# Performance work log

Hardware: AMD Instinct MI355X
Metric: run time of the kernel (lower is better)

## Reference

```python
import jax, jax.numpy as jnp
import numpy as np

N_HEAD = 16


def setup_inputs() -> dict:
    key = jax.random.key(0)
    ks = jax.random.split(key, 9)
    b, s, d = 4, 2048, 1024
    scale = 1.0 / np.sqrt(d)
    return {
        "x": jax.random.normal(ks[0], (b, s, d), dtype=jnp.float32),
        "Wq": jax.random.normal(ks[1], (d, d), dtype=jnp.float32) * scale,
        "bq": jax.random.normal(ks[2], (d,), dtype=jnp.float32) * 0.01,
        "Wk": jax.random.normal(ks[3], (d, d), dtype=jnp.float32) * scale,
        "bk": jax.random.normal(ks[4], (d,), dtype=jnp.float32) * 0.01,
        "Wv": jax.random.normal(ks[5], (d, d), dtype=jnp.float32) * scale,
        "bv": jax.random.normal(ks[6], (d,), dtype=jnp.float32) * 0.01,
        "Wo": jax.random.normal(ks[7], (d, d), dtype=jnp.float32) * scale,
        "bo": jax.random.normal(ks[8], (d,), dtype=jnp.float32) * 0.01,
        "mask": 1,
    }


def reference(x, Wq, bq, Wk, bk, Wv, bv, Wo, bo, mask):
    b, s, d = x.shape
    h = N_HEAD
    dh = d // h
    # projections -> [b, h, s, dh]
    def proj(W, bias):
        return (x @ W + bias).reshape(b, s, h, dh).transpose(0, 2, 1, 3)

    Q = proj(Wq, bq)
    K = proj(Wk, bk)
    V = proj(Wv, bv)

    # full S x S scores (module materializes them explicitly)
    scores = jnp.einsum('bhqd,bhkd->bhqk', Q, K)
    if mask:
        causal = jnp.triu(jnp.ones((s, s), dtype=bool), k=1)
        scores = jnp.where(causal, -jnp.inf, scores)
    scores = scores / jnp.sqrt(jnp.asarray(dh, dtype=scores.dtype))
    attn = jax.nn.softmax(scores, axis=-1)
    out = jnp.einsum('bhqk,bhkd->bhqd', attn, V)  # [b, h, s, dh]
    out = out.transpose(0, 2, 1, 3).reshape(b, s, d)
    return out @ Wo + bo
```

## Files before the change

### kernel.cpp

```cpp
#include <hip/hip_runtime.h>

typedef unsigned short u16;
typedef unsigned int u32;
typedef __bf16 bf16x8 __attribute__((ext_vector_type(8)));
typedef float f32x4 __attribute__((ext_vector_type(4)));

#define BATCH 4
#define SLEN 2048
#define DMODEL 1024
#define NHEAD 16
#define DHEAD 64
#define MROWS (BATCH * SLEN)

__device__ __forceinline__ u16 f32_to_bf16(float f) {
  u32 u = __float_as_uint(f);
  u32 r = (u + 0x7FFFu + ((u >> 16) & 1u)) >> 16;
  return (u16)r;
}
__device__ __forceinline__ u32 pack_bf16x2(float a, float b) {
  return (u32)f32_to_bf16(a) | ((u32)f32_to_bf16(b) << 16);
}

__device__ __forceinline__ u32 pack_trunc(float lo, float hi) {
#if __has_builtin(__builtin_amdgcn_perm)
  return __builtin_amdgcn_perm(__float_as_uint(hi), __float_as_uint(lo), 0x07060302u);
#else
  return (__float_as_uint(hi) & 0xFFFF0000u) | (__float_as_uint(lo) >> 16);
#endif
}
__device__ __forceinline__ u32 pack_round(float lo, float hi) {
  u32 ul = __float_as_uint(lo) + 0x8000u;
  u32 uh = __float_as_uint(hi) + 0x8000u;
#if __has_builtin(__builtin_amdgcn_perm)
  return __builtin_amdgcn_perm(uh, ul, 0x07060302u);
#else
  return (uh & 0xFFFF0000u) | (ul >> 16);
#endif
}

#if __has_builtin(__builtin_amdgcn_exp2f)
#define EXP2(x) __builtin_amdgcn_exp2f(x)
#else
#define EXP2(x) exp2f(x)
#endif

typedef const __attribute__((address_space(1))) void* gas_cv;
typedef __attribute__((address_space(3))) void* las_v;
__device__ __forceinline__ void async16(const u16* g, u16* l) {
  __builtin_amdgcn_global_load_lds((gas_cv)g, (las_v)l, 16, 0, 0);
}


__global__ void convert_x_kernel(const float* __restrict__ x, u16* __restrict__ xb) {
  size_t i = ((size_t)blockIdx.x * 256 + threadIdx.x) * 8;
  float4 v0 = *(const float4*)(x + i);
  float4 v1 = *(const float4*)(x + i + 4);
  uint4 o;
  o.x = pack_bf16x2(v0.x, v0.y);
  o.y = pack_bf16x2(v0.z, v0.w);
  o.z = pack_bf16x2(v1.x, v1.y);
  o.w = pack_bf16x2(v1.z, v1.w);
  *(uint4*)(xb + i) = o;
}

__global__ void transpose_w_kernel(const float* __restrict__ Wq, const float* __restrict__ Wk,
                                   const float* __restrict__ Wv, const float* __restrict__ Wo,
                                   u16* __restrict__ wqkvt, u16* __restrict__ wot) {
  __shared__ float tile[32][33];
  int z = blockIdx.z;
  const float* src = (z == 0) ? Wq : (z == 1) ? Wk : (z == 2) ? Wv : Wo;
  u16* dst = (z < 3) ? (wqkvt + (size_t)z * DMODEL * DMODEL) : wot;
  int c0 = blockIdx.x * 32, r0 = blockIdx.y * 32;
  int tx = threadIdx.x & 31, ty = threadIdx.x >> 5;
#pragma unroll
  for (int i = 0; i < 4; ++i)
    tile[ty + 8 * i][tx] = src[(size_t)(r0 + ty + 8 * i) * DMODEL + c0 + tx];
  __syncthreads();
#pragma unroll
  for (int i = 0; i < 4; ++i)
    dst[(size_t)(c0 + ty + 8 * i) * DMODEL + r0 + tx] = f32_to_bf16(tile[tx][ty + 8 * i]);
}

__global__ void concat_bias_kernel(const float* __restrict__ bq, const float* __restrict__ bk,
                                   const float* __restrict__ bv, float* __restrict__ bqkv) {
  int i = blockIdx.x * 256 + threadIdx.x;
  float v = (i < 1024) ? bq[i] : (i < 2048) ? bk[i - 1024] : bv[i - 2048];
  bqkv[i] = v;
}

__global__ void transpose_v_kernel(const u16* __restrict__ qkv, u16* __restrict__ vt) {
  __shared__ u16 tile[32][33];
  const int bh = blockIdx.z;
  const int b = bh >> 4, h = bh & 15;
  const int s0 = blockIdx.x * 32, d0 = blockIdx.y * 32;
  const int tx = threadIdx.x & 31, ty = threadIdx.x >> 5;
#pragma unroll
  for (int i = 0; i < 4; ++i)
    tile[ty + 8 * i][tx] =
        qkv[(size_t)(b * SLEN + s0 + ty + 8 * i) * (3 * DMODEL) + 2 * DMODEL + h * DHEAD + d0 + tx];
  __syncthreads();
#pragma unroll
  for (int i = 0; i < 4; ++i)
    vt[(size_t)(bh * DHEAD + d0 + ty + 8 * i) * SLEN + s0 + tx] = tile[tx][ty + 8 * i];
}

template <int OUT_BF16>
__global__ __launch_bounds__(256) void gemm_bt_kernel(const u16* __restrict__ A,
                                                      const u16* __restrict__ Bt,
                                                      const float* __restrict__ bias,
                                                      void* __restrict__ Cout,
                                                      int M, int N, int K) {
  __shared__ u16 sA[128 * 32];
  __shared__ u16 sB[128 * 32];
  const int tid = threadIdx.x;
  const int wv = tid >> 6, lane = tid & 63;
  const int wr = wv >> 1, wc = wv & 1;
  const int col = lane & 15, quad = lane >> 4;
  const int m0 = blockIdx.x * 128;
  const int n0 = blockIdx.y * 128;

  f32x4 acc[4][4] = {};

  const int lr = tid >> 2;
  const int ls = tid & 3;
  const size_t a_base = (size_t)(m0 + lr) * K + ls * 8;
  const size_t b_base = (size_t)(n0 + lr) * K + ls * 8;
  u16* ldsA0 = sA + ((tid >> 6) << 9);
  u16* ldsA1 = ldsA0 + 2048;
  u16* ldsB0 = sB + ((tid >> 6) << 9);
  u16* ldsB1 = ldsB0 + 2048;

  for (int k0 = 0; k0 < K; k0 += 32) {
    async16(A + a_base + k0, ldsA0);
    async16(A + a_base + (size_t)64 * K + k0, ldsA1);
    async16(Bt + b_base + k0, ldsB0);
    async16(Bt + b_base + (size_t)64 * K + k0, ldsB1);
    __syncthreads();
    bf16x8 af[4], bfr[4];
#pragma unroll
    for (int i = 0; i < 4; ++i)
      af[i] = *(const bf16x8*)(sA + (wr * 64 + i * 16 + col) * 32 + quad * 8);
#pragma unroll
    for (int j = 0; j < 4; ++j)
      bfr[j] = *(const bf16x8*)(sB + (wc * 64 + j * 16 + col) * 32 + quad * 8);
#pragma unroll
    for (int i = 0; i < 4; ++i)
#pragma unroll
      for (int j = 0; j < 4; ++j)
        acc[i][j] = __builtin_amdgcn_mfma_f32_16x16x32_bf16(af[i], bfr[j], acc[i][j], 0, 0, 0);
    __syncthreads();
  }

#pragma unroll
  for (int i = 0; i < 4; ++i) {
#pragma unroll
    for (int j = 0; j < 4; ++j) {
      int n = n0 + wc * 64 + j * 16 + col;
      float bia = bias[n];
#pragma unroll
      for (int r = 0; r < 4; ++r) {
        int m = m0 + wr * 64 + i * 16 + quad * 4 + r;
        float v = acc[i][j][r] + bia;
        if (OUT_BF16)
          ((u16*)Cout)[(size_t)m * N + n] = f32_to_bf16(v);
        else
          ((float*)Cout)[(size_t)m * N + n] = v;
      }
    }
  }
}

__global__ __launch_bounds__(256, 2) void attn_kernel(const u16* __restrict__ qkv,
                                                      const u16* __restrict__ vt,
                                                      u16* __restrict__ out) {
  const int bh = blockIdx.y;
  const int b = bh >> 4, h = bh & 15;
  const int tid = threadIdx.x;
  const int wv = tid >> 6, lane = tid & 63;
  const int col = lane & 15, quad = lane >> 4;
  const int bx = blockIdx.x;
  const int sfirst = bx * 4 + wv;

  __shared__ u16 sK[2][64 * 64];
  __shared__ u16 sV[2][64 * 64];
  __shared__ u16 sP[4][32 * 72];
  u16* mysP = sP[wv];

  const u16* kbase = qkv + ((size_t)(b * SLEN)) * (3 * DMODEL) + DMODEL + h * DHEAD;
  const u16* vbase = vt + ((size_t)bh * DHEAD) * SLEN;
  const float scl2 = 0.125f * 1.44269504088896f;

  const int lrow = lane >> 3;
  const int sga = (lane & 7) ^ lrow;
  const int r0a = wv * 16, r0b = wv * 16 + 8;
  const int swz = ((quad ) ^ (col & 7)) * 8;

  for (int half = 0; half < 2; ++half) {
    const int s2 = half ? (63 - sfirst) : sfirst;
    const int qbase = s2 * 32;
    const int nt_own = s2 / 2 + 1;
    const int nt_max = half ? (32 - 2 * bx) : (2 * bx + 2);

    const u16* qrow = qkv + ((size_t)(b * SLEN + qbase + col)) * (3 * DMODEL) + h * DHEAD;
    bf16x8 aQ[2][2];
#pragma unroll
    for (int i = 0; i < 2; ++i)
#pragma unroll
      for (int ks = 0; ks < 2; ++ks)
        aQ[i][ks] = *(const bf16x8*)(qrow + (size_t)i * 16 * (3 * DMODEL) + ks * 32 + quad * 8);

    f32x4 accO[2][4] = {};
    float m2[2] = {-1e30f, -1e30f}, l_i[2] = {0.0f, 0.0f};

    async16(kbase + (size_t)(r0a + lrow) * (3 * DMODEL) + sga * 8, sK[0] + r0a * 64);
    async16(kbase + (size_t)(r0b + lrow) * (3 * DMODEL) + sga * 8, sK[0] + r0b * 64);
    async16(vbase + (size_t)(r0a + lrow) * SLEN + sga * 8, sV[0] + r0a * 64);
    async16(vbase + (size_t)(r0b + lrow) * SLEN + sga * 8, sV[0] + r0b * 64);
    __syncthreads();

    for (int t = 0; t < nt_max; ++t) {
      const int kv0 = t * 64;
      const int cur = t & 1, nxt = cur ^ 1;

      if (t + 1 < nt_max) {
        const int kvn = kv0 + 64;
        async16(kbase + (size_t)(kvn + r0a + lrow) * (3 * DMODEL) + sga * 8, sK[nxt] + r0a * 64);
        async16(kbase + (size_t)(kvn + r0b + lrow) * (3 * DMODEL) + sga * 8, sK[nxt] + r0b * 64);
        async16(vbase + (size_t)(r0a + lrow) * SLEN + kvn + sga * 8, sV[nxt] + r0a * 64);
        async16(vbase + (size_t)(r0b + lrow) * SLEN + kvn + sga * 8, sV[nxt] + r0b * 64);
      }

      if (t < nt_own) {
        const u16* sKc = sK[cur];
        const u16* sVc = sV[cur];
        bf16x8 bK[2][4], bV[2][4];
#pragma unroll
        for (int ks = 0; ks < 2; ++ks) {
          const int sl = (((ks * 4 + quad) ^ (col & 7)) * 8);
#pragma unroll
          for (int cb = 0; cb < 4; ++cb)
            bK[ks][cb] = *(const bf16x8*)(sKc + (cb * 16 + col) * 64 + sl);
#pragma unroll
          for (int j = 0; j < 4; ++j)
            bV[ks][j] = *(const bf16x8*)(sVc + (j * 16 + col) * 64 + sl);
        }

        f32x4 accST[2][4] = {};
#pragma unroll
        for (int ks = 0; ks < 2; ++ks)
#pragma unroll
          for (int cb = 0; cb < 4; ++cb)
#pragma unroll
            for (int i = 0; i < 2; ++i)
              accST[i][cb] = __builtin_amdgcn_mfma_f32_16x16x32_bf16(bK[ks][cb], aQ[i][ks],
                                                                    accST[i][cb], 0, 0, 0);

        if (t == nt_own - 1) {
#pragma unroll
          for (int i = 0; i < 2; ++i) {
            int q = qbase + i * 16 + col;
#pragma unroll
            for (int cb = 0; cb < 4; ++cb) {
              int kvb = kv0 + cb * 16 + quad * 4;
#pragma unroll
              for (int r = 0; r < 4; ++r)
                if (kvb + r > q) accST[i][cb][r] = -1e30f;
            }
          }
        }

        float rmax[2], mnew[2], alpha[2], rsum[2];
#pragma unroll
        for (int i = 0; i < 2; ++i) {
          float m = accST[i][0][0];
#pragma unroll
          for (int cb = 0; cb < 4; ++cb)
#pragma unroll
            for (int r = 0; r < 4; ++r) m = fmaxf(m, accST[i][cb][r]);
          rmax[i] = m;
        }
#pragma unroll
        for (int i = 0; i < 2; ++i) {
          rmax[i] = fmaxf(rmax[i], __shfl_xor(rmax[i], 16));
          rmax[i] = fmaxf(rmax[i], __shfl_xor(rmax[i], 32));
          mnew[i] = fmaxf(m2[i], rmax[i] * scl2);
          alpha[i] = EXP2(m2[i] - mnew[i]);
          m2[i] = mnew[i];
        }
#pragma unroll
        for (int i = 0; i < 2; ++i) {
          float sacc = 0.0f;
#pragma unroll
          for (int cb = 0; cb < 4; ++cb)
#pragma unroll
            for (int r = 0; r < 4; ++r) {
              float p = EXP2(__builtin_fmaf(accST[i][cb][r], scl2, -mnew[i]));
              accST[i][cb][r] = p;
              sacc += p;
            }
          rsum[i] = sacc;
        }
#pragma unroll
        for (int i = 0; i < 2; ++i) {
          rsum[i] += __shfl_xor(rsum[i], 16);
          rsum[i] += __shfl_xor(rsum[i], 32);
          l_i[i] = l_i[i] * alpha[i] + rsum[i];
        }
#pragma unroll
        for (int i = 0; i < 2; ++i)
#pragma unroll
          for (int j = 0; j < 4; ++j)
#pragma unroll
            for (int r = 0; r < 4; ++r) accO[i][j][r] *= alpha[i];

#pragma unroll
        for (int i = 0; i < 2; ++i)
#pragma unroll
          for (int cb = 0; cb < 4; ++cb) {
            uint2 pk;
            pk.x = pack_trunc(accST[i][cb][0], accST[i][cb][1]);
            pk.y = pack_trunc(accST[i][cb][2], accST[i][cb][3]);
            *(uint2*)(mysP + (i * 16 + col) * 72 + cb * 16 + quad * 4) = pk;
          }
        bf16x8 aP[2][2];
#pragma unroll
        for (int i = 0; i < 2; ++i)
#pragma unroll
          for (int ks = 0; ks < 2; ++ks)
            aP[i][ks] = *(const bf16x8*)(mysP + (i * 16 + col) * 72 + ks * 32 + quad * 8);

#pragma unroll
        for (int ks = 0; ks < 2; ++ks)
#pragma unroll
          for (int j = 0; j < 4; ++j)
#pragma unroll
            for (int i = 0; i < 2; ++i)
              accO[i][j] = __builtin_amdgcn_mfma_f32_16x16x32_bf16(bV[ks][j], aP[i][ks],
                                                                  accO[i][j], 0, 0, 0);
      }

      __syncthreads();
    }

#pragma unroll
    for (int i = 0; i < 2; ++i) {
      float rl = 1.0f / l_i[i];
      size_t rowoff = ((size_t)(b * SLEN + qbase + i * 16 + col)) * DMODEL + h * DHEAD;
#pragma unroll
      for (int j = 0; j < 4; ++j) {
        uint2 pk;
        pk.x = pack_round(accO[i][j][0] * rl, accO[i][j][1] * rl);
        pk.y = pack_round(accO[i][j][2] * rl, accO[i][j][3] * rl);
        *(uint2*)(out + rowoff + j * 16 + quad * 4) = pk;
      }
    }
  }
}


extern "C" void kernel_launch(void* const* d_in, const int* in_sizes, int n_in,
                              void* d_out, int out_size, void* d_ws, size_t ws_size,
                              hipStream_t stream) {
  const float* x = (const float*)d_in[0];
  const float* Wq = (const float*)d_in[1];
  const float* bq = (const float*)d_in[2];
  const float* Wk = (const float*)d_in[3];
  const float* bk = (const float*)d_in[4];
  const float* Wv = (const float*)d_in[5];
  const float* bv = (const float*)d_in[6];
  const float* Wo = (const float*)d_in[7];
  const float* bo = (const float*)d_in[8];

  char* ws = (char*)d_ws;
  u16* xb = (u16*)ws;
  u16* wqkvt = (u16*)(ws + ((size_t)16 << 20));
  u16* wot = (u16*)(ws + ((size_t)22 << 20));
  u16* qkv = (u16*)(ws + ((size_t)24 << 20));
  u16* attnO = (u16*)(ws + ((size_t)72 << 20));
  float* bqkv = (float*)(ws + ((size_t)88 << 20));
  u16* vtp = xb;

  convert_x_kernel<<<4096, 256, 0, stream>>>(x, xb);
  transpose_w_kernel<<<dim3(32, 32, 4), 256, 0, stream>>>(Wq, Wk, Wv, Wo, wqkvt, wot);
  concat_bias_kernel<<<12, 256, 0, stream>>>(bq, bk, bv, bqkv);
  gemm_bt_kernel<1><<<dim3(64, 24), 256, 0, stream>>>(xb, wqkvt, bqkv, (void*)qkv,
                                                      MROWS, 3 * DMODEL, DMODEL);
  transpose_v_kernel<<<dim3(64, 2, 64), 256, 0, stream>>>(qkv, vtp);
  attn_kernel<<<dim3(8, BATCH * NHEAD), 256, 0, stream>>>(qkv, vtp, attnO);
  gemm_bt_kernel<0><<<dim3(64, 8), 256, 0, stream>>>(attnO, wot, bo, d_out,
                                                     MROWS, DMODEL, DMODEL);
}
```

Before: 286.3 us.

## Fuse V transpose into QKV GEMM epilogue, widen GEMM K-tile, re-split attention grid

The QKV projection GEMM now writes Q and K to a 2048-wide buffer and writes V directly in transposed per-head layout from its epilogue. This removes the separate transpose kernel and its extra read and write of V. The GEMM K-step grows from 32 to 64 and uses XOR-swizzled LDS to cut barriers and bank conflicts. Attention drops its two-half causal load balancing in favour of 16 blocks per head, launched heaviest-first with a launch-bounds hint of 3. This may lose load balance and adds register pressure.

```diff
diff --git a/kernel.cpp b/kernel.cpp
--- a/kernel.cpp
+++ b/kernel.cpp
@@ -11,6 +11,7 @@
 #define NHEAD 16
 #define DHEAD 64
 #define MROWS (BATCH * SLEN)
+#define QKS 2048
 
 __device__ __forceinline__ u16 f32_to_bf16(float f) {
   u32 u = __float_as_uint(f);
@@ -88,66 +89,49 @@
   bqkv[i] = v;
 }
 
-__global__ void transpose_v_kernel(const u16* __restrict__ qkv, u16* __restrict__ vt) {
-  __shared__ u16 tile[32][33];
-  const int bh = blockIdx.z;
-  const int b = bh >> 4, h = bh & 15;
-  const int s0 = blockIdx.x * 32, d0 = blockIdx.y * 32;
-  const int tx = threadIdx.x & 31, ty = threadIdx.x >> 5;
-#pragma unroll
-  for (int i = 0; i < 4; ++i)
-    tile[ty + 8 * i][tx] =
-        qkv[(size_t)(b * SLEN + s0 + ty + 8 * i) * (3 * DMODEL) + 2 * DMODEL + h * DHEAD + d0 + tx];
-  __syncthreads();
-#pragma unroll
-  for (int i = 0; i < 4; ++i)
-    vt[(size_t)(bh * DHEAD + d0 + ty + 8 * i) * SLEN + s0 + tx] = tile[tx][ty + 8 * i];
-}
-
-template <int OUT_BF16>
+
+#define GEMM_STAGE(Aptr, Bptr, k0)                                                     \
+  _Pragma("unroll") for (int c = 0; c < 4; ++c) {                                      \
+    const int rr = wv * 32 + c * 8;                                                    \
+    async16(Aptr + (size_t)(m0 + rr + lrow8) * K + (k0) + sga * 8, sA + rr * 64);      \
+    async16(Bptr + (size_t)(n0 + rr + lrow8) * K + (k0) + sga * 8, sB + rr * 64);      \
+  }
+
+#define GEMM_COMPUTE()                                                                 \
+  _Pragma("unroll") for (int ks = 0; ks < 2; ++ks) {                                   \
+    const int sl = ((ks * 4 + quad) ^ (col & 7)) * 8;                                  \
+    bf16x8 af[4], bfr[4];                                                              \
+    _Pragma("unroll") for (int i = 0; i < 4; ++i)                                      \
+        af[i] = *(const bf16x8*)(sA + (wr * 64 + i * 16 + col) * 64 + sl);             \
+    _Pragma("unroll") for (int j = 0; j < 4; ++j)                                      \
+        bfr[j] = *(const bf16x8*)(sB + (wc * 64 + j * 16 + col) * 64 + sl);            \
+    _Pragma("unroll") for (int i = 0; i < 4; ++i)                                      \
+        _Pragma("unroll") for (int j = 0; j < 4; ++j)                                  \
+            acc[i][j] = __builtin_amdgcn_mfma_f32_16x16x32_bf16(af[i], bfr[j],         \
+                                                                acc[i][j], 0, 0, 0);  \
+  }
+
 __global__ __launch_bounds__(256) void gemm_bt_kernel(const u16* __restrict__ A,
                                                       const u16* __restrict__ Bt,
                                                       const float* __restrict__ bias,
-                                                      void* __restrict__ Cout,
+                                                      float* __restrict__ Cout,
                                                       int M, int N, int K) {
-  __shared__ u16 sA[128 * 32];
-  __shared__ u16 sB[128 * 32];
+  __shared__ u16 sA[128 * 64];
+  __shared__ u16 sB[128 * 64];
   const int tid = threadIdx.x;
   const int wv = tid >> 6, lane = tid & 63;
   const int wr = wv >> 1, wc = wv & 1;
   const int col = lane & 15, quad = lane >> 4;
+  const int lrow8 = lane >> 3, sga = (lane & 7) ^ lrow8;
   const int m0 = blockIdx.x * 128;
   const int n0 = blockIdx.y * 128;
 
   f32x4 acc[4][4] = {};
 
-  const int lr = tid >> 2;
-  const int ls = tid & 3;
-  const size_t a_base = (size_t)(m0 + lr) * K + ls * 8;
-  const size_t b_base = (size_t)(n0 + lr) * K + ls * 8;
-  u16* ldsA0 = sA + ((tid >> 6) << 9);
-  u16* ldsA1 = ldsA0 + 2048;
-  u16* ldsB0 = sB + ((tid >> 6) << 9);
-  u16* ldsB1 = ldsB0 + 2048;
-
-  for (int k0 = 0; k0 < K; k0 += 32) {
-    async16(A + a_base + k0, ldsA0);
-    async16(A + a_base + (size_t)64 * K + k0, ldsA1);
-    async16(Bt + b_base + k0, ldsB0);
-    async16(Bt + b_base + (size_t)64 * K + k0, ldsB1);
+  for (int k0 = 0; k0 < K; k0 += 64) {
+    GEMM_STAGE(A, Bt, k0)
     __syncthreads();
-    bf16x8 af[4], bfr[4];
-#pragma unroll
-    for (int i = 0; i < 4; ++i)
-      af[i] = *(const bf16x8*)(sA + (wr * 64 + i * 16 + col) * 32 + quad * 8);
-#pragma unroll
-    for (int j = 0; j < 4; ++j)
-      bfr[j] = *(const bf16x8*)(sB + (wc * 64 + j * 16 + col) * 32 + quad * 8);
-#pragma unroll
-    for (int i = 0; i < 4; ++i)
-#pragma unroll
-      for (int j = 0; j < 4; ++j)
-        acc[i][j] = __builtin_amdgcn_mfma_f32_16x16x32_bf16(af[i], bfr[j], acc[i][j], 0, 0, 0);
+    GEMM_COMPUTE()
     __syncthreads();
   }
 
@@ -160,17 +144,72 @@
 #pragma unroll
       for (int r = 0; r < 4; ++r) {
         int m = m0 + wr * 64 + i * 16 + quad * 4 + r;
-        float v = acc[i][j][r] + bia;
-        if (OUT_BF16)
-          ((u16*)Cout)[(size_t)m * N + n] = f32_to_bf16(v);
-        else
-          ((float*)Cout)[(size_t)m * N + n] = v;
-      }
-    }
-  }
-}
-
-__global__ __launch_bounds__(256, 2) void attn_kernel(const u16* __restrict__ qkv,
+        Cout[(size_t)m * N + n] = acc[i][j][r] + bia;
+      }
+    }
+  }
+}
+
+__global__ __launch_bounds__(256) void gemm_qkv_kernel(const u16* __restrict__ A,
+                                                       const u16* __restrict__ Bt,
+                                                       const float* __restrict__ bias,
+                                                       u16* __restrict__ qk,
+                                                       u16* __restrict__ vt) {
+  const int K = DMODEL;
+  __shared__ u16 sA[128 * 64];
+  __shared__ u16 sB[128 * 64];
+  const int tid = threadIdx.x;
+  const int wv = tid >> 6, lane = tid & 63;
+  const int wr = wv >> 1, wc = wv & 1;
+  const int col = lane & 15, quad = lane >> 4;
+  const int lrow8 = lane >> 3, sga = (lane & 7) ^ lrow8;
+  const int m0 = blockIdx.x * 128;
+  const int n0 = blockIdx.y * 128;
+
+  f32x4 acc[4][4] = {};
+
+  for (int k0 = 0; k0 < K; k0 += 64) {
+    GEMM_STAGE(A, Bt, k0)
+    __syncthreads();
+    GEMM_COMPUTE()
+    __syncthreads();
+  }
+
+  if (n0 < 2048) {
+#pragma unroll
+    for (int i = 0; i < 4; ++i) {
+#pragma unroll
+      for (int j = 0; j < 4; ++j) {
+        int n = n0 + wc * 64 + j * 16 + col;
+        float bia = bias[n];
+#pragma unroll
+        for (int r = 0; r < 4; ++r) {
+          int m = m0 + wr * 64 + i * 16 + quad * 4 + r;
+          qk[(size_t)m * QKS + n] = f32_to_bf16(acc[i][j][r] + bia);
+        }
+      }
+    }
+  } else {
+#pragma unroll
+    for (int i = 0; i < 4; ++i) {
+      int m = m0 + wr * 64 + i * 16 + quad * 4;
+      int b = m >> 11, s = m & 2047;
+#pragma unroll
+      for (int j = 0; j < 4; ++j) {
+        int n = n0 + wc * 64 + j * 16 + col;
+        float bia = bias[n];
+        int hd = n - 2048;
+        size_t off = (size_t)((b << 10) | hd) * SLEN + s;
+        uint2 pk;
+        pk.x = pack_round(acc[i][j][0] + bia, acc[i][j][1] + bia);
+        pk.y = pack_round(acc[i][j][2] + bia, acc[i][j][3] + bia);
+        *(uint2*)(vt + off) = pk;
+      }
+    }
+  }
+}
+
+__global__ __launch_bounds__(256, 3) void attn_kernel(const u16* __restrict__ qk,
                                                       const u16* __restrict__ vt,
                                                       u16* __restrict__ out) {
   const int bh = blockIdx.y;
@@ -178,181 +217,176 @@
   const int tid = threadIdx.x;
   const int wv = tid >> 6, lane = tid & 63;
   const int col = lane & 15, quad = lane >> 4;
-  const int bx = blockIdx.x;
-  const int sfirst = bx * 4 + wv;
+  const int bxr = 15 - (int)blockIdx.x;
+  const int s2 = bxr * 4 + wv;
+  const int qbase = s2 * 32;
+  const int nt_own = s2 / 2 + 1;
+  const int nt_max = 2 * bxr + 2;
 
   __shared__ u16 sK[2][64 * 64];
   __shared__ u16 sV[2][64 * 64];
   __shared__ u16 sP[4][32 * 72];
   u16* mysP = sP[wv];
 
-  const u16* kbase = qkv + ((size_t)(b * SLEN)) * (3 * DMODEL) + DMODEL + h * DHEAD;
+  const u16* kbase = qk + ((size_t)(b * SLEN)) * QKS + 1024 + h * DHEAD;
   const u16* vbase = vt + ((size_t)bh * DHEAD) * SLEN;
   const float scl2 = 0.125f * 1.44269504088896f;
 
   const int lrow = lane >> 3;
   const int sga = (lane & 7) ^ lrow;
   const int r0a = wv * 16, r0b = wv * 16 + 8;
-  const int swz = ((quad ) ^ (col & 7)) * 8;
-
-  for (int half = 0; half < 2; ++half) {
-    const int s2 = half ? (63 - sfirst) : sfirst;
-    const int qbase = s2 * 32;
-    const int nt_own = s2 / 2 + 1;
-    const int nt_max = half ? (32 - 2 * bx) : (2 * bx + 2);
-
-    const u16* qrow = qkv + ((size_t)(b * SLEN + qbase + col)) * (3 * DMODEL) + h * DHEAD;
-    bf16x8 aQ[2][2];
-#pragma unroll
-    for (int i = 0; i < 2; ++i)
+
+  const u16* qrow = qk + ((size_t)(b * SLEN + qbase + col)) * QKS + h * DHEAD;
+  bf16x8 aQ[2][2];
+#pragma unroll
+  for (int i = 0; i < 2; ++i)
+#pragma unroll
+    for (int ks = 0; ks < 2; ++ks)
+      aQ[i][ks] = *(const bf16x8*)(qrow + (size_t)i * 16 * QKS + ks * 32 + quad * 8);
+
+  f32x4 accO[2][4] = {};
+  float m2[2] = {-1e30f, -1e30f}, l_i[2] = {0.0f, 0.0f};
+
+  async16(kbase + (size_t)(r0a + lrow) * QKS + sga * 8, sK[0] + r0a * 64);
+  async16(kbase + (size_t)(r0b + lrow) * QKS + sga * 8, sK[0] + r0b * 64);
+  async16(vbase + (size_t)(r0a + lrow) * SLEN + sga * 8, sV[0] + r0a * 64);
+  async16(vbase + (size_t)(r0b + lrow) * SLEN + sga * 8, sV[0] + r0b * 64);
+  __syncthreads();
+
+  for (int t = 0; t < nt_max; ++t) {
+    const int kv0 = t * 64;
+    const int cur = t & 1, nxt = cur ^ 1;
+
+    if (t + 1 < nt_max) {
+      const int kvn = kv0 + 64;
+      async16(kbase + (size_t)(kvn + r0a + lrow) * QKS + sga * 8, sK[nxt] + r0a * 64);
+      async16(kbase + (size_t)(kvn + r0b + lrow) * QKS + sga * 8, sK[nxt] + r0b * 64);
+      async16(vbase + (size_t)(r0a + lrow) * SLEN + kvn + sga * 8, sV[nxt] + r0a * 64);
+      async16(vbase + (size_t)(r0b + lrow) * SLEN + kvn + sga * 8, sV[nxt] + r0b * 64);
+    }
+
+    if (t < nt_own) {
+      const u16* sKc = sK[cur];
+      const u16* sVc = sV[cur];
+      bf16x8 bK[2][4], bV[2][4];
+#pragma unroll
+      for (int ks = 0; ks < 2; ++ks) {
+        const int sl = (((ks * 4 + quad) ^ (col & 7)) * 8);
+#pragma unroll
+        for (int cb = 0; cb < 4; ++cb)
+          bK[ks][cb] = *(const bf16x8*)(sKc + (cb * 16 + col) * 64 + sl);
+#pragma unroll
+        for (int j = 0; j < 4; ++j)
+          bV[ks][j] = *(const bf16x8*)(sVc + (j * 16 + col) * 64 + sl);
+      }
+
+      f32x4 accST[2][4] = {};
 #pragma unroll
       for (int ks = 0; ks < 2; ++ks)
-        aQ[i][ks] = *(const bf16x8*)(qrow + (size_t)i * 16 * (3 * DMODEL) + ks * 32 + quad * 8);
-
-    f32x4 accO[2][4] = {};
-    float m2[2] = {-1e30f, -1e30f}, l_i[2] = {0.0f, 0.0f};
-
-    async16(kbase + (size_t)(r0a + lrow) * (3 * DMODEL) + sga * 8, sK[0] + r0a * 64);
-    async16(kbase + (size_t)(r0b + lrow) * (3 * DMODEL) + sga * 8, sK[0] + r0b * 64);
-    async16(vbase + (size_t)(r0a + lrow) * SLEN + sga * 8, sV[0] + r0a * 64);
-    async16(vbase + (size_t)(r0b + lrow) * SLEN + sga * 8, sV[0] + r0b * 64);
-    __syncthreads();
-
-    for (int t = 0; t < nt_max; ++t) {
-      const int kv0 = t * 64;
-      const int cur = t & 1, nxt = cur ^ 1;
-
-      if (t + 1 < nt_max) {
-        const int kvn = kv0 + 64;
-        async16(kbase + (size_t)(kvn + r0a + lrow) * (3 * DMODEL) + sga * 8, sK[nxt] + r0a * 64);
-        async16(kbase + (size_t)(kvn + r0b + lrow) * (3 * DMODEL) + sga * 8, sK[nxt] + r0b * 64);
-        async16(vbase + (size_t)(r0a + lrow) * SLEN + kvn + sga * 8, sV[nxt] + r0a * 64);
-        async16(vbase + (size_t)(r0b + lrow) * SLEN + kvn + sga * 8, sV[nxt] + r0b * 64);
-      }
-
-      if (t < nt_own) {
-        const u16* sKc = sK[cur];
-        const u16* sVc = sV[cur];
-        bf16x8 bK[2][4], bV[2][4];
-#pragma unroll
-        for (int ks = 0; ks < 2; ++ks) {
-          const int sl = (((ks * 4 + quad) ^ (col & 7)) * 8);
-#pragma unroll
-          for (int cb = 0; cb < 4; ++cb)
-            bK[ks][cb] = *(const bf16x8*)(sKc + (cb * 16 + col) * 64 + sl);
-#pragma unroll
-          for (int j = 0; j < 4; ++j)
-            bV[ks][j] = *(const bf16x8*)(sVc + (j * 16 + col) * 64 + sl);
-        }
-
-        f32x4 accST[2][4] = {};
-#pragma unroll
-        for (int ks = 0; ks < 2; ++ks)
-#pragma unroll
-          for (int cb = 0; cb < 4; ++cb)
-#pragma unroll
-            for (int i = 0; i < 2; ++i)
-              accST[i][cb] = __builtin_amdgcn_mfma_f32_16x16x32_bf16(bK[ks][cb], aQ[i][ks],
-                                                                    accST[i][cb], 0, 0, 0);
-
-        if (t == nt_own - 1) {
-#pragma unroll
-          for (int i = 0; i < 2; ++i) {
-            int q = qbase + i * 16 + col;
-#pragma unroll
-            for (int cb = 0; cb < 4; ++cb) {
-              int kvb = kv0 + cb * 16 + quad * 4;
-#pragma unroll
-              for (int r = 0; r < 4; ++r)
-                if (kvb + r > q) accST[i][cb][r] = -1e30f;
-            }
+#pragma unroll
+        for (int cb = 0; cb < 4; ++cb)
+#pragma unroll
+          for (int i = 0; i < 2; ++i)
+            accST[i][cb] = __builtin_amdgcn_mfma_f32_16x16x32_bf16(bK[ks][cb], aQ[i][ks],
+                                                                  accST[i][cb], 0, 0, 0);
+
+      if (t == nt_own - 1) {
+#pragma unroll
+        for (int i = 0; i < 2; ++i) {
+          int q = qbase + i * 16 + col;
+#pragma unroll
+          for (int cb = 0; cb < 4; ++cb) {
+            int kvb = kv0 + cb * 16 + quad * 4;
+#pragma unroll
+            for (int r = 0; r < 4; ++r)
+              if (kvb + r > q) accST[i][cb][r] = -1e30f;
           }
         }
-
-        float rmax[2], mnew[2], alpha[2], rsum[2];
-#pragma unroll
-        for (int i = 0; i < 2; ++i) {
-          float m = accST[i][0][0];
-#pragma unroll
-          for (int cb = 0; cb < 4; ++cb)
-#pragma unroll
-            for (int r = 0; r < 4; ++r) m = fmaxf(m, accST[i][cb][r]);
-          rmax[i] = m;
+      }
+
+      float rmax[2], mnew[2], alpha[2], rsum[2];
+#pragma unroll
+      for (int i = 0; i < 2; ++i) {
+        float m = accST[i][0][0];
+#pragma unroll
+        for (int cb = 0; cb < 4; ++cb)
+#pragma unroll
+          for (int r = 0; r < 4; ++r) m = fmaxf(m, accST[i][cb][r]);
+        rmax[i] = m;
+      }
+#pragma unroll
+      for (int i = 0; i < 2; ++i) {
+        rmax[i] = fmaxf(rmax[i], __shfl_xor(rmax[i], 16));
+        rmax[i] = fmaxf(rmax[i], __shfl_xor(rmax[i], 32));
+        mnew[i] = fmaxf(m2[i], rmax[i] * scl2);
+        alpha[i] = EXP2(m2[i] - mnew[i]);
+        m2[i] = mnew[i];
+      }
+#pragma unroll
+      for (int i = 0; i < 2; ++i) {
+        float sacc = 0.0f;
+#pragma unroll
+        for (int cb = 0; cb < 4; ++cb)
+#pragma unroll
+          for (int r = 0; r < 4; ++r) {
+            float p = EXP2(__builtin_fmaf(accST[i][cb][r], scl2, -mnew[i]));
+            accST[i][cb][r] = p;
+            sacc += p;
+          }
+        rsum[i] = sacc;
+      }
+#pragma unroll
+      for (int i = 0; i < 2; ++i) {
+        rsum[i] += __shfl_xor(rsum[i], 16);
+        rsum[i] += __shfl_xor(rsum[i], 32);
+        l_i[i] = l_i[i] * alpha[i] + rsum[i];
+      }
+#pragma unroll
+      for (int i = 0; i < 2; ++i)
+#pragma unroll
+        for (int j = 0; j < 4; ++j)
+#pragma unroll
+          for (int r = 0; r < 4; ++r) accO[i][j][r] *= alpha[i];
+
+#pragma unroll
+      for (int i = 0; i < 2; ++i)
+#pragma unroll
+        for (int cb = 0; cb < 4; ++cb) {
+          uint2 pk;
+          pk.x = pack_trunc(accST[i][cb][0], accST[i][cb][1]);
+          pk.y = pack_trunc(accST[i][cb][2], accST[i][cb][3]);
+          *(uint2*)(mysP + (i * 16 + col) * 72 + cb * 16 + quad * 4) = pk;
         }
-#pragma unroll
-        for (int i = 0; i < 2; ++i) {
-          rmax[i] = fmaxf(rmax[i], __shfl_xor(rmax[i], 16));
-          rmax[i] = fmaxf(rmax[i], __shfl_xor(rmax[i], 32));
-          mnew[i] = fmaxf(m2[i], rmax[i] * scl2);
-          alpha[i] = EXP2(m2[i] - mnew[i]);
-          m2[i] = mnew[i];
-        }
-#pragma unroll
-        for (int i = 0; i < 2; ++i) {
-          float sacc = 0.0f;
-#pragma unroll
-          for (int cb = 0; cb < 4; ++cb)
-#pragma unroll
-            for (int r = 0; r < 4; ++r) {
-              float p = EXP2(__builtin_fmaf(accST[i][cb][r], scl2, -mnew[i]));
-              accST[i][cb][r] = p;
-              sacc += p;
-            }
-          rsum[i] = sacc;
-        }
-#pragma unroll
-        for (int i = 0; i < 2; ++i) {
-          rsum[i] += __shfl_xor(rsum[i], 16);
-          rsum[i] += __shfl_xor(rsum[i], 32);
-          l_i[i] = l_i[i] * alpha[i] + rsum[i];
-        }
-#pragma unroll
-        for (int i = 0; i < 2; ++i)
-#pragma unroll
-          for (int j = 0; j < 4; ++j)
-#pragma unroll
-            for (int r = 0; r < 4; ++r) accO[i][j][r] *= alpha[i];
-
-#pragma unroll
-        for (int i = 0; i < 2; ++i)
-#pragma unroll
-          for (int cb = 0; cb < 4; ++cb) {
-            uint2 pk;
-            pk.x = pack_trunc(accST[i][cb][0], accST[i][cb][1]);
-            pk.y = pack_trunc(accST[i][cb][2], accST[i][cb][3]);
-            *(uint2*)(mysP + (i * 16 + col) * 72 + cb * 16 + quad * 4) = pk;
-          }
-        bf16x8 aP[2][2];
-#pragma unroll
-        for (int i = 0; i < 2; ++i)
-#pragma unroll
-          for (int ks = 0; ks < 2; ++ks)
-            aP[i][ks] = *(const bf16x8*)(mysP + (i * 16 + col) * 72 + ks * 32 + quad * 8);
-
+      bf16x8 aP[2][2];
+#pragma unroll
+      for (int i = 0; i < 2; ++i)
 #pragma unroll
         for (int ks = 0; ks < 2; ++ks)
-#pragma unroll
-          for (int j = 0; j < 4; ++j)
-#pragma unroll
-            for (int i = 0; i < 2; ++i)
-              accO[i][j] = __builtin_amdgcn_mfma_f32_16x16x32_bf16(bV[ks][j], aP[i][ks],
-                                                                  accO[i][j], 0, 0, 0);
-      }
-
-      __syncthreads();
-    }
-
-#pragma unroll
-    for (int i = 0; i < 2; ++i) {
-      float rl = 1.0f / l_i[i];
-      size_t rowoff = ((size_t)(b * SLEN + qbase + i * 16 + col)) * DMODEL + h * DHEAD;
-#pragma unroll
-      for (int j = 0; j < 4; ++j) {
-        uint2 pk;
-        pk.x = pack_round(accO[i][j][0] * rl, accO[i][j][1] * rl);
-        pk.y = pack_round(accO[i][j][2] * rl, accO[i][j][3] * rl);
-        *(uint2*)(out + rowoff + j * 16 + quad * 4) = pk;
-      }
+          aP[i][ks] = *(const bf16x8*)(mysP + (i * 16 + col) * 72 + ks * 32 + quad * 8);
+
+#pragma unroll
+      for (int ks = 0; ks < 2; ++ks)
+#pragma unroll
+        for (int j = 0; j < 4; ++j)
+#pragma unroll
+          for (int i = 0; i < 2; ++i)
+            accO[i][j] = __builtin_amdgcn_mfma_f32_16x16x32_bf16(bV[ks][j], aP[i][ks],
+                                                                accO[i][j], 0, 0, 0);
+    }
+
+    __syncthreads();
+  }
+
+#pragma unroll
+  for (int i = 0; i < 2; ++i) {
+    float rl = 1.0f / l_i[i];
+    size_t rowoff = ((size_t)(b * SLEN + qbase + i * 16 + col)) * DMODEL + h * DHEAD;
+#pragma unroll
+    for (int j = 0; j < 4; ++j) {
+      uint2 pk;
+      pk.x = pack_round(accO[i][j][0] * rl, accO[i][j][1] * rl);
+      pk.y = pack_round(accO[i][j][2] * rl, accO[i][j][3] * rl);
+      *(uint2*)(out + rowoff + j * 16 + quad * 4) = pk;
     }
   }
 }
@@ -375,18 +409,16 @@
   u16* xb = (u16*)ws;
   u16* wqkvt = (u16*)(ws + ((size_t)16 << 20));
   u16* wot = (u16*)(ws + ((size_t)22 << 20));
-  u16* qkv = (u16*)(ws + ((size_t)24 << 20));
+  u16* qk = (u16*)(ws + ((size_t)24 << 20));
+  u16* vtp = (u16*)(ws + ((size_t)56 << 20));
   u16* attnO = (u16*)(ws + ((size_t)72 << 20));
   float* bqkv = (float*)(ws + ((size_t)88 << 20));
-  u16* vtp = xb;
 
   convert_x_kernel<<<4096, 256, 0, stream>>>(x, xb);
   transpose_w_kernel<<<dim3(32, 32, 4), 256, 0, stream>>>(Wq, Wk, Wv, Wo, wqkvt, wot);
   concat_bias_kernel<<<12, 256, 0, stream>>>(bq, bk, bv, bqkv);
-  gemm_bt_kernel<1><<<dim3(64, 24), 256, 0, stream>>>(xb, wqkvt, bqkv, (void*)qkv,
-                                                      MROWS, 3 * DMODEL, DMODEL);
-  transpose_v_kernel<<<dim3(64, 2, 64), 256, 0, stream>>>(qkv, vtp);
-  attn_kernel<<<dim3(8, BATCH * NHEAD), 256, 0, stream>>>(qkv, vtp, attnO);
-  gemm_bt_kernel<0><<<dim3(64, 8), 256, 0, stream>>>(attnO, wot, bo, d_out,
-                                                     MROWS, DMODEL, DMODEL);
-}
+  gemm_qkv_kernel<<<dim3(64, 24), 256, 0, stream>>>(xb, wqkvt, bqkv, qk, vtp);
+  attn_kernel<<<dim3(16, BATCH * NHEAD), 256, 0, stream>>>(qk, vtp, attnO);
+  gemm_bt_kernel<<<dim3(64, 8), 256, 0, stream>>>(attnO, wot, bo, (float*)d_out,
+                                                  MROWS, DMODEL, DMODEL);
+}
```

Result: slower. 302.9 us (+5.8%).
